# Kernel tuning notes

Hardware: AMD Instinct MI355X
Metric: run time of the kernel (lower is better)

## Reference

```python
import jax, jax.numpy as jnp
import numpy as np

N_NODES = 100000
N_EDGES = 150000
D_IN = 512
D_HID = 512
N_GRAPHS = 64


def setup_inputs() -> dict:
    key = jax.random.key(0)
    ks = jax.random.split(key, 12)
    x = jax.random.normal(ks[0], (N_NODES, D_IN), dtype=jnp.float32)
    edge_index = jax.random.randint(ks[1], (2, N_EDGES), 0, N_NODES, dtype=jnp.int64)
    batch = jnp.sort(jax.random.randint(ks[2], (N_NODES,), 0, N_GRAPHS, dtype=jnp.int64))
    s1 = 1.0 / np.sqrt(D_IN)
    s2 = 1.0 / np.sqrt(D_HID)
    # GINConv layer 1: MLP([D_IN, D_HID, D_HID])
    W1a = jax.random.uniform(ks[3], (D_IN, D_HID), jnp.float32, -s1, s1)
    b1a = jax.random.uniform(ks[4], (D_HID,), jnp.float32, -s1, s1)
    W1b = jax.random.uniform(ks[5], (D_HID, D_HID), jnp.float32, -s2, s2)
    b1b = jax.random.uniform(ks[6], (D_HID,), jnp.float32, -s2, s2)
    # GINConv layer 2 (out_channels=1): MLP([D_HID, 1, 1])
    W2a = jax.random.uniform(ks[7], (D_HID, 1), jnp.float32, -s2, s2)
    b2a = jax.random.uniform(ks[8], (1,), jnp.float32, -s2, s2)
    W2b = jax.random.uniform(ks[9], (1, 1), jnp.float32, -1.0, 1.0)
    b2b = jax.random.uniform(ks[10], (1,), jnp.float32, -1.0, 1.0)
    return {"x": x, "edge_index": edge_index, "batch": batch,
            "W1a": W1a, "b1a": b1a, "W1b": W1b, "b1b": b1b,
            "W2a": W2a, "b2a": b2a, "W2b": W2b, "b2b": b2b}


def _gin_conv(h, src, dst, Wa, ba, Wb, bb):
    # sum-aggregate neighbor features, add (1+eps)*x with eps=0, then MLP
    agg = jax.ops.segment_sum(h[src], dst, num_segments=N_NODES)  # [N, d]
    z = agg + h
    z = jnp.maximum(jnp.dot(z, Wa) + ba, 0.0)  # Linear -> ReLU
    return jnp.dot(z, Wb) + bb                  # Linear (plain last)


def reference(x, edge_index, batch, W1a, b1a, W1b, b1b, W2a, b2a, W2b, b2b):
    src, dst = edge_index[0], edge_index[1]
    h = _gin_conv(x, src, dst, W1a, b1a, W1b, b1b)
    h = jnp.maximum(h, 0.0)  # inter-layer activation (not applied after last layer)
    h = _gin_conv(h, src, dst, W2a, b2a, W2b, b2b)  # [N, 1]
    # global mean pool over graph assignment
    sums = jax.ops.segment_sum(h, batch, num_segments=N_GRAPHS)  # [G, 1]
    cnt = jax.ops.segment_sum(jnp.ones((N_NODES, 1), h.dtype), batch, num_segments=N_GRAPHS)
    return sums / jnp.maximum(cnt, 1.0)
```

## Files before the change

kernel.cpp:

```cpp
#include <hip/hip_runtime.h>
#include <hip/hip_bf16.h>

#define N_NODES_C 100000
#define N_EDGES_C 150000
#define DC 512
#define NG 64

typedef float f32x4 __attribute__((ext_vector_type(4)));
typedef short s16x8 __attribute__((ext_vector_type(8)));
typedef short s16x4 __attribute__((ext_vector_type(4)));

__device__ __forceinline__ short f2bf(float f) {
    union { float f; unsigned u; } c; c.f = f;
    unsigned r = c.u + 0x7fffu + ((c.u >> 16) & 1u);
    return (short)(r >> 16);
}


__global__ void zero_k(float* s, float* aggs, int* cnt, float* gsum, float* gcnt) {
    int i = blockIdx.x * 256 + threadIdx.x;
    if (i < N_NODES_C) { s[i] = 0.f; aggs[i] = 0.f; cnt[i] = 0; }
    if (i < NG) { gsum[i] = 0.f; gcnt[i] = 0.f; }
}

__global__ void transpose_w(const float* __restrict__ in, short* __restrict__ out) {
    __shared__ float tile[32][33];
    int tx = threadIdx.x & 31;
    int ty = threadIdx.x >> 5;
    int k0 = blockIdx.y * 32;
    int n0 = blockIdx.x * 32;
#pragma unroll
    for (int i = 0; i < 4; ++i)
        tile[ty + i * 8][tx] = in[(size_t)(k0 + ty + i * 8) * DC + n0 + tx];
    __syncthreads();
#pragma unroll
    for (int i = 0; i < 4; ++i)
        out[(size_t)(n0 + ty + i * 8) * DC + k0 + tx] = f2bf(tile[tx][ty + i * 8]);
}


__global__ void hist_k(const int* __restrict__ ei, int* __restrict__ cnt) {
    int e = blockIdx.x * 256 + threadIdx.x;
    if (e < N_EDGES_C) atomicAdd(&cnt[ei[N_EDGES_C + e]], 1);
}

__global__ void scan1_k(const int* __restrict__ cnt, int* __restrict__ off,
                        int* __restrict__ bsum) {
    __shared__ int sh[1024];
    int tid = threadIdx.x;
    int i = blockIdx.x * 1024 + tid;
    int v = (i < N_NODES_C) ? cnt[i] : 0;
    sh[tid] = v;
    __syncthreads();
    for (int d = 1; d < 1024; d <<= 1) {
        int t = (tid >= d) ? sh[tid - d] : 0;
        __syncthreads();
        sh[tid] += t;
        __syncthreads();
    }
    if (i < N_NODES_C) off[i] = sh[tid] - v;
    if (tid == 1023) bsum[blockIdx.x] = sh[1023];
}

#define NSCAN_BLK 98

__global__ void scan2_k(int* __restrict__ bsum) {
    __shared__ int sh[128];
    int tid = threadIdx.x;
    int v = (tid < NSCAN_BLK) ? bsum[tid] : 0;
    sh[tid] = v;
    __syncthreads();
    for (int d = 1; d < 128; d <<= 1) {
        int t = (tid >= d) ? sh[tid - d] : 0;
        __syncthreads();
        sh[tid] += t;
        __syncthreads();
    }
    if (tid < NSCAN_BLK) bsum[tid] = sh[tid] - v;
}

__global__ void scan3_k(int* __restrict__ off, const int* __restrict__ bsum) {
    int i = blockIdx.x * 1024 + threadIdx.x;
    if (i < N_NODES_C) off[i] += bsum[blockIdx.x];
}

__global__ void place_k(const int* __restrict__ ei, int* __restrict__ off,
                        int* __restrict__ ssrc) {
    int e = blockIdx.x * 256 + threadIdx.x;
    if (e < N_EDGES_C) {
        int d = ei[N_EDGES_C + e];
        int p = atomicAdd(&off[d], 1);
        ssrc[p] = ei[e];
    }
}

__global__ void gather_k(const float* __restrict__ x, const int* __restrict__ off,
                         const int* __restrict__ ssrc, short* __restrict__ zb) {
    int node = blockIdx.x * 2 + (threadIdx.x >> 7);
    if (node >= N_NODES_C) return;
    int t = threadIdx.x & 127;
    int beg = (node == 0) ? 0 : off[node - 1];
    int end = off[node];
    f32x4 acc = *(const f32x4*)(x + (size_t)node * DC + t * 4);
    for (int j = beg; j < end; ++j) {
        int s = ssrc[j];
        acc += *(const f32x4*)(x + (size_t)s * DC + t * 4);
    }
    s16x4 r;
    r.x = f2bf(acc.x); r.y = f2bf(acc.y); r.z = f2bf(acc.z); r.w = f2bf(acc.w);
    *(s16x4*)(zb + (size_t)node * DC + t * 4) = r;
}


__global__ void edge_scalar(const int* __restrict__ ei, const float* __restrict__ s,
                            float* __restrict__ aggs) {
    int e = blockIdx.x * 256 + threadIdx.x;
    if (e < N_EDGES_C) atomicAdd(&aggs[ei[N_EDGES_C + e]], s[ei[e]]);
}

__global__ void node_pool(const float* __restrict__ s, const float* __restrict__ aggs,
                          const int* __restrict__ batch, const float* __restrict__ b2a,
                          float* __restrict__ gsum, float* __restrict__ gcnt) {
    __shared__ float ls[NG], lc[NG];
    int t = threadIdx.x;
    if (t < NG) { ls[t] = 0.f; lc[t] = 0.f; }
    __syncthreads();
    int i = blockIdx.x * 256 + t;
    if (i < N_NODES_C) {
        float z2 = fmaxf(aggs[i] + s[i] + b2a[0], 0.0f);
        int g = batch[i];
        atomicAdd(&ls[g], z2);
        atomicAdd(&lc[g], 1.0f);
    }
    __syncthreads();
    if (t < NG && lc[t] != 0.f) {
        atomicAdd(&gsum[t], ls[t]);
        atomicAdd(&gcnt[t], lc[t]);
    }
}

__global__ void finalize_k(const float* gsum, const float* gcnt, const float* w2b,
                           const float* b2b, float* out) {
    int g = threadIdx.x;
    if (g < NG) {
        float c = fmaxf(gcnt[g], 1.0f);
        out[g] = gsum[g] / c * w2b[0] + b2b[0];
    }
}

#define BM 128
#define BN 128
#define BK 32
#define LDK 40

template <int EPI>
__global__ __launch_bounds__(256, 2) void gemm_k(const short* __restrict__ A,
                                                 const short* __restrict__ Bt,
                                                 const float* __restrict__ bias,
                                                 short* __restrict__ Cout,
                                                 const float* __restrict__ w2a,
                                                 float* __restrict__ s_out) {
    __shared__ alignas(16) short As[BM * LDK];
    __shared__ alignas(16) short Bs[BN * LDK];

    const int tid  = threadIdx.x;
    const int brow = blockIdx.y * BM;
    const int bcol = blockIdx.x * BN;

    const int lane = tid & 63;
    const int wr   = (tid >> 7) * 64;
    const int wc   = ((tid >> 6) & 1) * 64;
    const int lr   = lane & 15;
    const int lk   = (lane >> 4) * 8;

    f32x4 acc[4][4] = {};

    const int str = tid >> 1;
    const int skk = (tid & 1) * 16;
    int arow = brow + str;
    if (arow >= N_NODES_C) arow = N_NODES_C - 1;

    const short* agp = A + (size_t)arow * DC + skk;
    const short* bgp = Bt + (size_t)(bcol + str) * DC + skk;

    for (int kt = 0; kt < DC / BK; ++kt) {
        const int k0 = kt * BK;
        s16x8 a0 = *(const s16x8*)(agp + k0);
        s16x8 a1 = *(const s16x8*)(agp + k0 + 8);
        s16x8 b0 = *(const s16x8*)(bgp + k0);
        s16x8 b1 = *(const s16x8*)(bgp + k0 + 8);

        __syncthreads();
        *(s16x8*)&As[str * LDK + skk + 0] = a0;
        *(s16x8*)&As[str * LDK + skk + 8] = a1;
        *(s16x8*)&Bs[str * LDK + skk + 0] = b0;
        *(s16x8*)&Bs[str * LDK + skk + 8] = b1;
        __syncthreads();

        s16x8 af[4], bfr[4];
#pragma unroll
        for (int mi = 0; mi < 4; ++mi)
            af[mi] = *(const s16x8*)&As[(wr + mi * 16 + lr) * LDK + lk];
#pragma unroll
        for (int ni = 0; ni < 4; ++ni)
            bfr[ni] = *(const s16x8*)&Bs[(wc + ni * 16 + lr) * LDK + lk];
#pragma unroll
        for (int mi = 0; mi < 4; ++mi)
#pragma unroll
            for (int ni = 0; ni < 4; ++ni)
                acc[mi][ni] = __builtin_amdgcn_mfma_f32_16x16x32_bf16(af[mi], bfr[ni],
                                                                      acc[mi][ni], 0, 0, 0);
    }

    const int rb = brow + wr + (lane >> 4) * 4;
    const int cb = bcol + wc + lr;

    if constexpr (EPI == 0) {
        float bv[4];
#pragma unroll
        for (int ni = 0; ni < 4; ++ni) bv[ni] = bias[cb + ni * 16];
#pragma unroll
        for (int mi = 0; mi < 4; ++mi) {
#pragma unroll
            for (int r = 0; r < 4; ++r) {
                int row = rb + mi * 16 + r;
                if (row < N_NODES_C) {
#pragma unroll
                    for (int ni = 0; ni < 4; ++ni) {
                        float v = fmaxf(acc[mi][ni][r] + bv[ni], 0.0f);
                        Cout[(size_t)row * DC + cb + ni * 16] = f2bf(v);
                    }
                }
            }
        }
    } else {
        float bv[4], wv[4];
#pragma unroll
        for (int ni = 0; ni < 4; ++ni) {
            bv[ni] = bias[cb + ni * 16];
            wv[ni] = w2a[cb + ni * 16];
        }
#pragma unroll
        for (int mi = 0; mi < 4; ++mi) {
#pragma unroll
            for (int r = 0; r < 4; ++r) {
                float sum = 0.f;
#pragma unroll
                for (int ni = 0; ni < 4; ++ni) {
                    float v = fmaxf(acc[mi][ni][r] + bv[ni], 0.0f);
                    sum += v * wv[ni];
                }
#pragma unroll
                for (int off = 1; off < 16; off <<= 1) sum += __shfl_xor(sum, off, 64);
                int row = rb + mi * 16 + r;
                if (lr == 0 && row < N_NODES_C) atomicAdd(&s_out[row], sum);
            }
        }
    }
}


extern "C" void kernel_launch(void* const* d_in, const int* in_sizes, int n_in,
                              void* d_out, int out_size, void* d_ws, size_t ws_size,
                              hipStream_t stream) {
    const float* x     = (const float*)d_in[0];
    const int*   ei    = (const int*)d_in[1];
    const int*   batch = (const int*)d_in[2];
    const float* b1a   = (const float*)d_in[4];
    const float* b1b   = (const float*)d_in[6];
    const float* W2a   = (const float*)d_in[7];
    const float* b2a   = (const float*)d_in[8];
    const float* W2b   = (const float*)d_in[9];
    const float* b2b   = (const float*)d_in[10];
    const float* W1a   = (const float*)d_in[3];
    const float* W1b   = (const float*)d_in[5];
    float* out = (float*)d_out;

    char* w = (char*)d_ws;
    short* zb   = (short*)(w);
    short* z1   = (short*)(w + 102400000);
    short* WT1  = (short*)(w + 204800000);
    short* WT2  = (short*)(w + 205324288);
    float* sbuf = (float*)(w + 205848576);
    float* aggs = (float*)(w + 206248576);
    int*   cnt  = (int*)  (w + 206648576);
    int*   offb = (int*)  (w + 207048576);
    int*   ssrc = (int*)  (w + 207448576);
    int*   bsum = (int*)  (w + 208048576);
    float* gsum = (float*)(w + 208049088);
    float* gcnt = (float*)(w + 208049344);

    zero_k<<<391, 256, 0, stream>>>(sbuf, aggs, cnt, gsum, gcnt);
    transpose_w<<<dim3(16, 16), 256, 0, stream>>>(W1a, WT1);
    transpose_w<<<dim3(16, 16), 256, 0, stream>>>(W1b, WT2);

    hist_k<<<586, 256, 0, stream>>>(ei, cnt);
    scan1_k<<<NSCAN_BLK, 1024, 0, stream>>>(cnt, offb, bsum);
    scan2_k<<<1, 128, 0, stream>>>(bsum);
    scan3_k<<<NSCAN_BLK, 1024, 0, stream>>>(offb, bsum);
    place_k<<<586, 256, 0, stream>>>(ei, offb, ssrc);
    gather_k<<<50000, 256, 0, stream>>>(x, offb, ssrc, zb);

    gemm_k<0><<<dim3(4, 782), 256, 0, stream>>>(zb, WT1, b1a, z1, nullptr, nullptr);
    gemm_k<1><<<dim3(4, 782), 256, 0, stream>>>(z1, WT2, b1b, nullptr, W2a, sbuf);

    edge_scalar<<<586, 256, 0, stream>>>(ei, sbuf, aggs);
    node_pool<<<391, 256, 0, stream>>>(sbuf, aggs, batch, b2a, gsum, gcnt);
    finalize_k<<<1, 64, 0, stream>>>(gsum, gcnt, W2b, b2b, out);
}
```

Before: 340.1 us.

## Apply first linear before neighbor aggregation and gather bf16 projected features

Uses linearity ((A+I)x)W = (A+I)(xW) to run the first GEMM directly on fp32 x, converting to bf16 while loading into shared memory, and only then aggregate the projected rows. The gather now reads bf16 rows of y (half the bytes of fp32 x) and fuses bias add and ReLU, which removes the fp32 gather pass and the intermediate zb write/read. The trade-off is that neighbor sums are now taken over bf16-rounded GEMM outputs rather than rounded after summing, which changes numerics slightly, and the GEMM A-load now reads fp32 and converts inline.

```diff
diff --git a/kernel.cpp b/kernel.cpp
--- a/kernel.cpp
+++ b/kernel.cpp
@@ -14,6 +14,11 @@
     union { float f; unsigned u; } c; c.f = f;
     unsigned r = c.u + 0x7fffu + ((c.u >> 16) & 1u);
     return (short)(r >> 16);
+}
+__device__ __forceinline__ float bf2f(short v) {
+    union { unsigned u; float f; } c;
+    c.u = ((unsigned)(unsigned short)v) << 16;
+    return c.f;
 }
 
 
@@ -94,21 +99,46 @@
     }
 }
 
-__global__ void gather_k(const float* __restrict__ x, const int* __restrict__ off,
-                         const int* __restrict__ ssrc, short* __restrict__ zb) {
-    int node = blockIdx.x * 2 + (threadIdx.x >> 7);
+__global__ void gather_relu_k(const short* __restrict__ y, const int* __restrict__ off,
+                              const int* __restrict__ ssrc, const float* __restrict__ b1a,
+                              short* __restrict__ z1) {
+    int node = blockIdx.x * 4 + (threadIdx.x >> 6);
     if (node >= N_NODES_C) return;
-    int t = threadIdx.x & 127;
+    int t = threadIdx.x & 63;
+    const int col = t * 8;
     int beg = (node == 0) ? 0 : off[node - 1];
     int end = off[node];
-    f32x4 acc = *(const f32x4*)(x + (size_t)node * DC + t * 4);
-    for (int j = beg; j < end; ++j) {
-        int s = ssrc[j];
-        acc += *(const f32x4*)(x + (size_t)s * DC + t * 4);
-    }
-    s16x4 r;
-    r.x = f2bf(acc.x); r.y = f2bf(acc.y); r.z = f2bf(acc.z); r.w = f2bf(acc.w);
-    *(s16x4*)(zb + (size_t)node * DC + t * 4) = r;
+    s16x8 own = *(const s16x8*)(y + (size_t)node * DC + col);
+    float acc[8];
+#pragma unroll
+    for (int q = 0; q < 8; ++q) acc[q] = bf2f(own[q]);
+    int j = beg;
+    for (; j + 2 <= end; j += 2) {
+        int s0 = ssrc[j];
+        int s1 = ssrc[j + 1];
+        s16x8 r0 = *(const s16x8*)(y + (size_t)s0 * DC + col);
+        s16x8 r1 = *(const s16x8*)(y + (size_t)s1 * DC + col);
+#pragma unroll
+        for (int q = 0; q < 8; ++q) acc[q] += bf2f(r0[q]) + bf2f(r1[q]);
+    }
+    if (j < end) {
+        int s0 = ssrc[j];
+        s16x8 r0 = *(const s16x8*)(y + (size_t)s0 * DC + col);
+#pragma unroll
+        for (int q = 0; q < 8; ++q) acc[q] += bf2f(r0[q]);
+    }
+    f32x4 bv0 = *(const f32x4*)(b1a + col);
+    f32x4 bv1 = *(const f32x4*)(b1a + col + 4);
+    s16x8 o;
+    o[0] = f2bf(fmaxf(acc[0] + bv0.x, 0.f));
+    o[1] = f2bf(fmaxf(acc[1] + bv0.y, 0.f));
+    o[2] = f2bf(fmaxf(acc[2] + bv0.z, 0.f));
+    o[3] = f2bf(fmaxf(acc[3] + bv0.w, 0.f));
+    o[4] = f2bf(fmaxf(acc[4] + bv1.x, 0.f));
+    o[5] = f2bf(fmaxf(acc[5] + bv1.y, 0.f));
+    o[6] = f2bf(fmaxf(acc[6] + bv1.z, 0.f));
+    o[7] = f2bf(fmaxf(acc[7] + bv1.w, 0.f));
+    *(s16x8*)(z1 + (size_t)node * DC + col) = o;
 }
 
 
@@ -153,8 +183,8 @@
 #define BK 32
 #define LDK 40
 
-template <int EPI>
-__global__ __launch_bounds__(256, 2) void gemm_k(const short* __restrict__ A,
+template <int ASRC, int EPI>
+__global__ __launch_bounds__(256, 2) void gemm_k(const void* __restrict__ Ap,
                                                  const short* __restrict__ Bt,
                                                  const float* __restrict__ bias,
                                                  short* __restrict__ Cout,
@@ -180,19 +210,32 @@
     int arow = brow + str;
     if (arow >= N_NODES_C) arow = N_NODES_C - 1;
 
-    const short* agp = A + (size_t)arow * DC + skk;
     const short* bgp = Bt + (size_t)(bcol + str) * DC + skk;
 
     for (int kt = 0; kt < DC / BK; ++kt) {
         const int k0 = kt * BK;
-        s16x8 a0 = *(const s16x8*)(agp + k0);
-        s16x8 a1 = *(const s16x8*)(agp + k0 + 8);
+        short areg[16];
+        if constexpr (ASRC == 0) {
+            const float* ap = (const float*)Ap + (size_t)arow * DC + k0 + skk;
+            f32x4 a0 = *(const f32x4*)(ap + 0);
+            f32x4 a1 = *(const f32x4*)(ap + 4);
+            f32x4 a2 = *(const f32x4*)(ap + 8);
+            f32x4 a3 = *(const f32x4*)(ap + 12);
+            areg[0]  = f2bf(a0.x); areg[1]  = f2bf(a0.y); areg[2]  = f2bf(a0.z); areg[3]  = f2bf(a0.w);
+            areg[4]  = f2bf(a1.x); areg[5]  = f2bf(a1.y); areg[6]  = f2bf(a1.z); areg[7]  = f2bf(a1.w);
+            areg[8]  = f2bf(a2.x); areg[9]  = f2bf(a2.y); areg[10] = f2bf(a2.z); areg[11] = f2bf(a2.w);
+            areg[12] = f2bf(a3.x); areg[13] = f2bf(a3.y); areg[14] = f2bf(a3.z); areg[15] = f2bf(a3.w);
+        } else {
+            const short* ap = (const short*)Ap + (size_t)arow * DC + k0 + skk;
+            *(s16x8*)&areg[0] = *(const s16x8*)(ap + 0);
+            *(s16x8*)&areg[8] = *(const s16x8*)(ap + 8);
+        }
         s16x8 b0 = *(const s16x8*)(bgp + k0);
         s16x8 b1 = *(const s16x8*)(bgp + k0 + 8);
 
         __syncthreads();
-        *(s16x8*)&As[str * LDK + skk + 0] = a0;
-        *(s16x8*)&As[str * LDK + skk + 8] = a1;
+        *(s16x8*)&As[str * LDK + skk + 0] = *(s16x8*)&areg[0];
+        *(s16x8*)&As[str * LDK + skk + 8] = *(s16x8*)&areg[8];
         *(s16x8*)&Bs[str * LDK + skk + 0] = b0;
         *(s16x8*)&Bs[str * LDK + skk + 8] = b1;
         __syncthreads();
@@ -215,10 +258,12 @@
     const int rb = brow + wr + (lane >> 4) * 4;
     const int cb = bcol + wc + lr;
 
-    if constexpr (EPI == 0) {
-        float bv[4];
-#pragma unroll
-        for (int ni = 0; ni < 4; ++ni) bv[ni] = bias[cb + ni * 16];
+    if constexpr (EPI == 0 || EPI == 2) {
+        float bv[4] = {0.f, 0.f, 0.f, 0.f};
+        if constexpr (EPI == 0) {
+#pragma unroll
+            for (int ni = 0; ni < 4; ++ni) bv[ni] = bias[cb + ni * 16];
+        }
 #pragma unroll
         for (int mi = 0; mi < 4; ++mi) {
 #pragma unroll
@@ -227,7 +272,8 @@
                 if (row < N_NODES_C) {
 #pragma unroll
                     for (int ni = 0; ni < 4; ++ni) {
-                        float v = fmaxf(acc[mi][ni][r] + bv[ni], 0.0f);
+                        float v = acc[mi][ni][r] + bv[ni];
+                        if constexpr (EPI == 0) v = fmaxf(v, 0.0f);
                         Cout[(size_t)row * DC + cb + ni * 16] = f2bf(v);
                     }
                 }
@@ -266,18 +312,18 @@
     const float* x     = (const float*)d_in[0];
     const int*   ei    = (const int*)d_in[1];
     const int*   batch = (const int*)d_in[2];
+    const float* W1a   = (const float*)d_in[3];
     const float* b1a   = (const float*)d_in[4];
+    const float* W1b   = (const float*)d_in[5];
     const float* b1b   = (const float*)d_in[6];
     const float* W2a   = (const float*)d_in[7];
     const float* b2a   = (const float*)d_in[8];
     const float* W2b   = (const float*)d_in[9];
     const float* b2b   = (const float*)d_in[10];
-    const float* W1a   = (const float*)d_in[3];
-    const float* W1b   = (const float*)d_in[5];
     float* out = (float*)d_out;
 
     char* w = (char*)d_ws;
-    short* zb   = (short*)(w);
+    short* y    = (short*)(w);
     short* z1   = (short*)(w + 102400000);
     short* WT1  = (short*)(w + 204800000);
     short* WT2  = (short*)(w + 205324288);
@@ -299,10 +345,10 @@
     scan2_k<<<1, 128, 0, stream>>>(bsum);
     scan3_k<<<NSCAN_BLK, 1024, 0, stream>>>(offb, bsum);
     place_k<<<586, 256, 0, stream>>>(ei, offb, ssrc);
-    gather_k<<<50000, 256, 0, stream>>>(x, offb, ssrc, zb);
-
-    gemm_k<0><<<dim3(4, 782), 256, 0, stream>>>(zb, WT1, b1a, z1, nullptr, nullptr);
-    gemm_k<1><<<dim3(4, 782), 256, 0, stream>>>(z1, WT2, b1b, nullptr, W2a, sbuf);
+
+    gemm_k<0, 2><<<dim3(4, 782), 256, 0, stream>>>(x, WT1, nullptr, y, nullptr, nullptr);
+    gather_relu_k<<<25000, 256, 0, stream>>>(y, offb, ssrc, b1a, z1);
+    gemm_k<1, 1><<<dim3(4, 782), 256, 0, stream>>>(z1, WT2, b1b, nullptr, W2a, sbuf);
 
     edge_scalar<<<586, 256, 0, stream>>>(ei, sbuf, aggs);
     node_pool<<<391, 256, 0, stream>>>(sbuf, aggs, batch, b2a, gsum, gcnt);
```

Result: no change. 340.9 us (+0.2%).
